# Kernel optimization log

Measured on AMD Instinct MI355X. Metric: run time of the kernel, lower is better.

Reference implementation:

```python
import jax, jax.numpy as jnp
import numpy as np
import math

B, S, IN_DIM, ORIG_DIM, EMBED, HEADS = 8, 1024, 512, 64, 512, 8
HEAD_DIM = EMBED // HEADS


def setup_inputs() -> dict:
    key = jax.random.key(0)
    ks = jax.random.split(key, 4)
    # xavier-uniform-ish init for weights, zero bias (matches _reset_parameters)
    def xavier(k, shape):
        fan_in, fan_out = shape[1], shape[0]
        lim = math.sqrt(6.0 / (fan_in + fan_out))
        return jax.random.uniform(k, shape, jnp.float32, -lim, lim)
    return {
        "x": jax.random.normal(ks[0], (B, S, IN_DIM), jnp.float32),
        "inp": jax.random.normal(ks[1], (B, S, ORIG_DIM), jnp.float32),
        "W_qkv": xavier(ks[2], (3 * EMBED, IN_DIM + ORIG_DIM)),
        "b_qkv": jnp.zeros((3 * EMBED,), jnp.float32),
        "W_o": xavier(ks[3], (EMBED, EMBED)),
        "b_o": jnp.zeros((EMBED,), jnp.float32),
    }


def reference(x, inp, W_qkv, b_qkv, W_o, b_o):
    b, s, _ = x.shape
    xc = jnp.concatenate([x, inp], axis=2)              # [B,S,IN+ORIG]
    qkv = xc @ W_qkv.T + b_qkv                          # [B,S,3E]
    qkv = qkv.reshape(b, s, HEADS, 3 * HEAD_DIM).transpose(0, 2, 1, 3)  # [B,H,S,3d]
    q, k, v = jnp.split(qkv, 3, axis=-1)                # each [B,H,S,d]
    logits = jnp.einsum("bhqd,bhkd->bhqk", q, k) / math.sqrt(HEAD_DIM)
    attention = jax.nn.softmax(logits, axis=-1)         # [B,H,S,S]
    values = jnp.einsum("bhqk,bhkd->bhqd", attention, v)
    values = values.transpose(0, 2, 1, 3).reshape(b, s, EMBED)
    o = values @ W_o.T + b_o                            # [B,S,E]
    return o, attention
```

## Files before the change

### kernel.cpp

```cpp
#include <hip/hip_runtime.h>

typedef __bf16 bf16x8 __attribute__((ext_vector_type(8)));
typedef __bf16 bf16x4 __attribute__((ext_vector_type(4)));
typedef float f32x4 __attribute__((ext_vector_type(4)));

#define MFMA16(a,b,c) __builtin_amdgcn_mfma_f32_16x16x32_bf16((a),(b),(c),0,0,0)

__device__ __forceinline__ float fexp2(float x) { return __builtin_amdgcn_exp2f(x); }

__device__ __forceinline__ void gload_lds16(const void* g, void* l) {
    __builtin_amdgcn_global_load_lds(
        (const __attribute__((address_space(1))) void*)g,
        (__attribute__((address_space(3))) void*)l, 16, 0, 0);
}


__global__ __launch_bounds__(256) void k_convert(
    const float* __restrict__ x, const float* __restrict__ inp,
    const float* __restrict__ Wqkv, const float* __restrict__ Wo,
    __bf16* __restrict__ xc, __bf16* __restrict__ wq, __bf16* __restrict__ wo)
{
    const unsigned C1 = 589824u;
    const unsigned C2 = 110592u;
    unsigned i = blockIdx.x * 256u + threadIdx.x;
    if (i < C1) {
        unsigned e = i * 8u;
        unsigned m = e / 576u, k = e - m * 576u;
        const float* p = (k < 512u) ? x + (size_t)m * 512u + k
                                    : inp + (size_t)m * 64u + (k - 512u);
        f32x4 a = *(const f32x4*)p, b = *(const f32x4*)(p + 4);
        bf16x8 o;
#pragma unroll
        for (int j = 0; j < 4; ++j) { o[j] = (__bf16)a[j]; o[j + 4] = (__bf16)b[j]; }
        *(bf16x8*)&xc[e] = o;
    } else if (i < C1 + C2) {
        unsigned e = (i - C1) * 8u;
        f32x4 a = *(const f32x4*)&Wqkv[e], b = *(const f32x4*)&Wqkv[e + 4];
        bf16x8 o;
#pragma unroll
        for (int j = 0; j < 4; ++j) { o[j] = (__bf16)a[j]; o[j + 4] = (__bf16)b[j]; }
        *(bf16x8*)&wq[e] = o;
    } else {
        unsigned e = (i - C1 - C2) * 8u;
        f32x4 a = *(const f32x4*)&Wo[e], b = *(const f32x4*)&Wo[e + 4];
        bf16x8 o;
#pragma unroll
        for (int j = 0; j < 4; ++j) { o[j] = (__bf16)a[j]; o[j + 4] = (__bf16)b[j]; }
        *(bf16x8*)&wo[e] = o;
    }
}

__global__ __launch_bounds__(256) void k_qkv_gemm(
    const __bf16* __restrict__ A, const __bf16* __restrict__ W,
    const float* __restrict__ bias,
    __bf16* __restrict__ q_ws, __bf16* __restrict__ k_ws, __bf16* __restrict__ vt_ws)
{
    const int K = 576;
    __shared__ __align__(16) char smem[17408];
    __bf16 (*As)[32] = (__bf16 (*)[32])smem;
    __bf16 (*Bs)[32] = (__bf16 (*)[32])(smem + 8192);
    int m0 = blockIdx.x * 128, n0 = blockIdx.y * 128;
    int t = threadIdx.x, w = t >> 6, l = t & 63;
    int lo = l & 15, hi = l >> 4;
    int wr = w >> 1, wc = w & 1;

    const __bf16* gA = A + (size_t)(m0 + w * 16 + (l >> 2)) * K + (l & 3) * 8;
    const __bf16* gB = W + (size_t)(n0 + w * 16 + (l >> 2)) * K + (l & 3) * 8;
    char* lA = smem + w * 1024;
    char* lB = smem + 8192 + w * 1024;

    float bias_reg[4];
#pragma unroll
    for (int ni = 0; ni < 4; ++ni) bias_reg[ni] = bias[n0 + wc * 64 + ni * 16 + lo];

    f32x4 acc[4][4] = {};
    for (int k0 = 0; k0 < K; k0 += 32) {
        gload_lds16(gA + k0, lA);
        gload_lds16(gA + 64 * K + k0, lA + 4096);
        gload_lds16(gB + k0, lB);
        gload_lds16(gB + 64 * K + k0, lB + 4096);
        __syncthreads();
        bf16x8 af[4], bq[4];
#pragma unroll
        for (int mi = 0; mi < 4; ++mi) af[mi] = *(const bf16x8*)&As[wr * 64 + mi * 16 + lo][hi * 8];
#pragma unroll
        for (int ni = 0; ni < 4; ++ni) bq[ni] = *(const bf16x8*)&Bs[wc * 64 + ni * 16 + lo][hi * 8];
#pragma unroll
        for (int mi = 0; mi < 4; ++mi)
#pragma unroll
            for (int ni = 0; ni < 4; ++ni)
                acc[mi][ni] = MFMA16(af[mi], bq[ni], acc[mi][ni]);
        __syncthreads();
    }

    int q64 = (n0 >> 6) + wc;
    int head = q64 / 3, part = q64 - head * 3;
    int mbase = m0 + wr * 64;
    size_t bh = (size_t)((mbase >> 10) * 8 + head);
    int sbase = mbase & 1023;

    if (part < 2) {
        float scale = (part == 0) ? 0.180336881f : 1.0f;
        __bf16* dst = (part == 0 ? q_ws : k_ws) + (bh * 1024 + sbase) * 64;
        __bf16 (*Ep)[68] = (__bf16 (*)[68])(smem + w * 4352);
#pragma unroll
        for (int hh = 0; hh < 2; ++hh) {
#pragma unroll
            for (int mi2 = 0; mi2 < 2; ++mi2) {
                int mi = hh * 2 + mi2;
#pragma unroll
                for (int ni = 0; ni < 4; ++ni)
#pragma unroll
                    for (int j = 0; j < 4; ++j)
                        Ep[mi2 * 16 + hi * 4 + j][ni * 16 + lo] =
                            (__bf16)((acc[mi][ni][j] + bias_reg[ni]) * scale);
            }
#pragma unroll
            for (int it = 0; it < 4; ++it) {
                int r = it * 8 + (l >> 3);
                bf16x8 v = *(const bf16x8*)&Ep[r][(l & 7) * 8];
                *(bf16x8*)&dst[(size_t)(hh * 32 + r) * 64 + (l & 7) * 8] = v;
            }
        }
    } else {
        __bf16* dst = vt_ws + bh * 65536 + sbase;
        __bf16 (*Ep)[34] = (__bf16 (*)[34])(smem + w * 4352);
#pragma unroll
        for (int hh = 0; hh < 2; ++hh) {
#pragma unroll
            for (int mi2 = 0; mi2 < 2; ++mi2) {
                int mi = hh * 2 + mi2;
#pragma unroll
                for (int ni = 0; ni < 4; ++ni)
#pragma unroll
                    for (int j = 0; j < 4; ++j)
                        Ep[ni * 16 + lo][mi2 * 16 + hi * 4 + j] =
                            (__bf16)(acc[mi][ni][j] + bias_reg[ni]);
            }
#pragma unroll
            for (int it = 0; it < 4; ++it) {
                int d = it * 16 + (l >> 2);
                bf16x8 v = *(const bf16x8*)&Ep[d][(l & 3) * 8];
                *(bf16x8*)&dst[(size_t)d * 1024 + hh * 32 + (l & 3) * 8] = v;
            }
        }
    }
}

__global__ __launch_bounds__(256, 4) void k_attn(
    const __bf16* __restrict__ q_ws, const __bf16* __restrict__ k_ws,
    const __bf16* __restrict__ vt_ws,
    float* __restrict__ att_out, __bf16* __restrict__ values)
{
    __shared__ __align__(16) __bf16 Klds[2][64][76];
    __shared__ __align__(16) __bf16 Pl[2][4][16][76];

    int bid = blockIdx.x;
    int nid = (bid & 7) * 128 + (bid >> 3);
    int bh = nid >> 4, qt = nid & 15;
    int t = threadIdx.x, w = t >> 6, l = t & 63;
    int lo = l & 15, hi = l >> 4;
    int q0 = qt * 64 + w * 16;

    const __bf16* Qg = q_ws + ((size_t)bh * 1024 + q0 + lo) * 64 + hi * 8;
    bf16x8 qa0 = *(const bf16x8*)Qg;
    bf16x8 qa1 = *(const bf16x8*)(Qg + 32);

    const __bf16* Kb = k_ws + (size_t)bh * 65536;
    int srow = t >> 2, scol = (t & 3) * 16;
    const __bf16* gK = Kb + (size_t)srow * 64 + scol;
    bf16x8 r0, r1;

#define STAGE_LOAD(c)  { const __bf16* p_ = gK + (size_t)(c) * 4096; \
                         r0 = *(const bf16x8*)p_; r1 = *(const bf16x8*)(p_ + 8); }
#define STAGE_WRITE(b) { *(bf16x8*)&Klds[b][srow][scol] = r0; \
                         *(bf16x8*)&Klds[b][srow][scol + 8] = r1; }
#define SCHUNK(b, s)   _Pragma("unroll") \
                       for (int kk = 0; kk < 4; ++kk) { \
                           bf16x8 kb0 = *(const bf16x8*)&Klds[b][kk * 16 + lo][hi * 8]; \
                           bf16x8 kb1 = *(const bf16x8*)&Klds[b][kk * 16 + lo][hi * 8 + 32]; \
                           f32x4 a_ = {}; \
                           a_ = MFMA16(qa0, kb0, a_); \
                           a_ = MFMA16(qa1, kb1, a_); \
                           s[kk] = a_; \
                       }

    f32x4 lmx = { -3.4e38f, -3.4e38f, -3.4e38f, -3.4e38f };
    f32x4 lsum = {};
    STAGE_LOAD(0); STAGE_WRITE(0);
    __syncthreads();
    for (int c = 0; c < 16; ++c) {
        if (c < 15) STAGE_LOAD(c + 1);
        f32x4 s[4];
        SCHUNK(c & 1, s);
#pragma unroll
        for (int j = 0; j < 4; ++j) {
            float cm = fmaxf(fmaxf(s[0][j], s[1][j]), fmaxf(s[2][j], s[3][j]));
            float nm = fmaxf(lmx[j], cm);
            float a = fexp2(s[0][j] - nm) + fexp2(s[1][j] - nm)
                    + fexp2(s[2][j] - nm) + fexp2(s[3][j] - nm);
            lsum[j] = lsum[j] * fexp2(lmx[j] - nm) + a;
            lmx[j] = nm;
        }
        if (c < 15) STAGE_WRITE((c + 1) & 1);
        __syncthreads();
    }
    f32x4 gmx = lmx;
#pragma unroll
    for (int off = 1; off < 16; off <<= 1)
#pragma unroll
        for (int j = 0; j < 4; ++j) gmx[j] = fmaxf(gmx[j], __shfl_xor(gmx[j], off));
    f32x4 part;
#pragma unroll
    for (int j = 0; j < 4; ++j) part[j] = lsum[j] * fexp2(lmx[j] - gmx[j]);
#pragma unroll
    for (int off = 1; off < 16; off <<= 1)
#pragma unroll
        for (int j = 0; j < 4; ++j) part[j] += __shfl_xor(part[j], off);
    f32x4 ginv;
#pragma unroll
    for (int j = 0; j < 4; ++j) ginv[j] = 1.f / part[j];

    float* gattW = att_out + ((size_t)bh * 1024 + q0) * 1024;
    const __bf16* Vb = vt_ws + (size_t)bh * 65536 + (size_t)(w * 16 + lo) * 1024 + hi * 8;
    f32x4 oacc[4] = {};

    STAGE_LOAD(0); STAGE_WRITE(0);
    __syncthreads();
    for (int c = 0; c < 16; ++c) {
        if (c < 15) STAGE_LOAD(c + 1);
        f32x4 s[4];
        SCHUNK(c & 1, s);
#pragma unroll
        for (int kk = 0; kk < 4; ++kk)
#pragma unroll
            for (int j = 0; j < 4; ++j) {
                float p = fexp2(s[kk][j] - gmx[j]) * ginv[j];
                gattW[(size_t)(hi * 4 + j) * 1024 + c * 64 + kk * 16 + lo] = p;
                Pl[c & 1][w][hi * 4 + j][kk * 16 + lo] = (__bf16)p;
            }
        if (c > 0) {
            int pb = (c - 1) & 1;
            const __bf16* vp = Vb + (size_t)(c - 1) * 64;
            bf16x8 vb0 = *(const bf16x8*)vp;
            bf16x8 vb1 = *(const bf16x8*)(vp + 32);
#pragma unroll
            for (int g = 0; g < 4; ++g) {
                bf16x8 pa0 = *(const bf16x8*)&Pl[pb][g][lo][hi * 8];
                bf16x8 pa1 = *(const bf16x8*)&Pl[pb][g][lo][hi * 8 + 32];
                oacc[g] = MFMA16(pa0, vb0, oacc[g]);
                oacc[g] = MFMA16(pa1, vb1, oacc[g]);
            }
        }
        if (c < 15) STAGE_WRITE((c + 1) & 1);
        __syncthreads();
    }
    {
        const __bf16* vp = Vb + (size_t)15 * 64;
        bf16x8 vb0 = *(const bf16x8*)vp;
        bf16x8 vb1 = *(const bf16x8*)(vp + 32);
#pragma unroll
        for (int g = 0; g < 4; ++g) {
            bf16x8 pa0 = *(const bf16x8*)&Pl[1][g][lo][hi * 8];
            bf16x8 pa1 = *(const bf16x8*)&Pl[1][g][lo][hi * 8 + 32];
            oacc[g] = MFMA16(pa0, vb0, oacc[g]);
            oacc[g] = MFMA16(pa1, vb1, oacc[g]);
        }
    }

    int b = bh >> 3, h = bh & 7;
#pragma unroll
    for (int g = 0; g < 4; ++g)
#pragma unroll
        for (int j = 0; j < 4; ++j)
            values[((size_t)b * 1024 + qt * 64 + g * 16 + hi * 4 + j) * 512
                   + h * 64 + w * 16 + lo] = (__bf16)oacc[g][j];
#undef STAGE_LOAD
#undef STAGE_WRITE
#undef SCHUNK
}

__global__ __launch_bounds__(256) void k_out_gemm(
    const __bf16* __restrict__ A, const __bf16* __restrict__ W,
    const float* __restrict__ bias, float* __restrict__ out)
{
    const int K = 512;
    __shared__ __align__(16) __bf16 As[128][32];
    __shared__ __align__(16) __bf16 Bs[128][32];
    int m0 = blockIdx.x * 128, n0 = blockIdx.y * 128;
    int t = threadIdx.x, w = t >> 6, l = t & 63;
    int lo = l & 15, hi = l >> 4;
    int wr = w >> 1, wc = w & 1;

    const __bf16* gA = A + (size_t)(m0 + w * 16 + (l >> 2)) * K + (l & 3) * 8;
    const __bf16* gB = W + (size_t)(n0 + w * 16 + (l >> 2)) * K + (l & 3) * 8;
    char* lA = (char*)&As[0][0] + w * 1024;
    char* lB = (char*)&Bs[0][0] + w * 1024;

    f32x4 acc[4][4] = {};
    for (int k0 = 0; k0 < K; k0 += 32) {
        gload_lds16(gA + k0, lA);
        gload_lds16(gA + 64 * K + k0, lA + 4096);
        gload_lds16(gB + k0, lB);
        gload_lds16(gB + 64 * K + k0, lB + 4096);
        __syncthreads();
        bf16x8 af[4], bq[4];
#pragma unroll
        for (int mi = 0; mi < 4; ++mi) af[mi] = *(const bf16x8*)&As[wr * 64 + mi * 16 + lo][hi * 8];
#pragma unroll
        for (int ni = 0; ni < 4; ++ni) bq[ni] = *(const bf16x8*)&Bs[wc * 64 + ni * 16 + lo][hi * 8];
#pragma unroll
        for (int mi = 0; mi < 4; ++mi)
#pragma unroll
            for (int ni = 0; ni < 4; ++ni)
                acc[mi][ni] = MFMA16(af[mi], bq[ni], acc[mi][ni]);
        __syncthreads();
    }

#pragma unroll
    for (int ni = 0; ni < 4; ++ni) {
        int n = n0 + wc * 64 + ni * 16 + lo;
        float bn = bias[n];
#pragma unroll
        for (int mi = 0; mi < 4; ++mi)
#pragma unroll
            for (int j = 0; j < 4; ++j) {
                int m = m0 + wr * 64 + mi * 16 + hi * 4 + j;
                out[(size_t)m * 512 + n] = acc[mi][ni][j] + bn;
            }
    }
}

extern "C" void kernel_launch(void* const* d_in, const int* in_sizes, int n_in,
                              void* d_out, int out_size, void* d_ws, size_t ws_size,
                              hipStream_t stream)
{
    const float* x    = (const float*)d_in[0];
    const float* inp  = (const float*)d_in[1];
    const float* Wqkv = (const float*)d_in[2];
    const float* bqkv = (const float*)d_in[3];
    const float* Wo   = (const float*)d_in[4];
    const float* bo   = (const float*)d_in[5];

    float* out_o   = (float*)d_out;
    float* out_att = out_o + (size_t)8 * 1024 * 512;

    char* ws = (char*)d_ws;
    __bf16* xc    = (__bf16*)(ws + 0);
    __bf16* wq    = (__bf16*)(ws + 9437184);
    __bf16* wo    = (__bf16*)(ws + 11206656);
    __bf16* q_ws  = (__bf16*)(ws + 11730944);
    __bf16* k_ws  = (__bf16*)(ws + 20119552);
    __bf16* vt_ws = (__bf16*)(ws + 28508160);
    __bf16* vals  = (__bf16*)(ws + 36896768);

    k_convert<<<2864, 256, 0, stream>>>(x, inp, Wqkv, Wo, xc, wq, wo);
    k_qkv_gemm<<<dim3(64, 12), 256, 0, stream>>>(xc, wq, bqkv, q_ws, k_ws, vt_ws);
    k_attn<<<1024, 256, 0, stream>>>(q_ws, k_ws, vt_ws, out_att, vals);
    k_out_gemm<<<dim3(64, 4), 256, 0, stream>>>(vals, wo, bo, out_o);
}
```

Baseline: 126.7 us.

## Double K-step per iteration and XOR-swizzle LDS tiles in QKV GEMM

The QKV projection GEMM now stages a 64-wide K slice per iteration instead of 32, which halves the number of barrier pairs, and grows LDS from about 17 KB to 32 KB. Tile rows are stored with an XOR swizzle on the 16-byte chunk index, applied on both the global-to-LDS load addresses and the fragment reads, to avoid LDS bank conflicts. The larger LDS footprint may lower occupancy, and K=576 must divide evenly by 64, which it does.

```diff
diff --git a/kernel.cpp b/kernel.cpp
--- a/kernel.cpp
+++ b/kernel.cpp
@@ -56,40 +56,51 @@
     __bf16* __restrict__ q_ws, __bf16* __restrict__ k_ws, __bf16* __restrict__ vt_ws)
 {
     const int K = 576;
-    __shared__ __align__(16) char smem[17408];
-    __bf16 (*As)[32] = (__bf16 (*)[32])smem;
-    __bf16 (*Bs)[32] = (__bf16 (*)[32])(smem + 8192);
+    __shared__ __align__(16) char smem[32768];
     int m0 = blockIdx.x * 128, n0 = blockIdx.y * 128;
     int t = threadIdx.x, w = t >> 6, l = t & 63;
     int lo = l & 15, hi = l >> 4;
     int wr = w >> 1, wc = w & 1;
 
-    const __bf16* gA = A + (size_t)(m0 + w * 16 + (l >> 2)) * K + (l & 3) * 8;
-    const __bf16* gB = W + (size_t)(n0 + w * 16 + (l >> 2)) * K + (l & 3) * 8;
-    char* lA = smem + w * 1024;
-    char* lB = smem + 8192 + w * 1024;
+    int srow = w * 8 + (l >> 3);
+    unsigned xswz = ((unsigned)((l & 7) * 16)) ^ (((unsigned)(l >> 3)) << 4);
+    const char* gA = (const char*)(A + (size_t)(m0 + srow) * K) + xswz;
+    const char* gB = (const char*)(W + (size_t)(n0 + srow) * K) + xswz;
 
     float bias_reg[4];
 #pragma unroll
     for (int ni = 0; ni < 4; ++ni) bias_reg[ni] = bias[n0 + wc * 64 + ni * 16 + lo];
 
+    unsigned xm = ((unsigned)(lo & 7)) << 4;
     f32x4 acc[4][4] = {};
-    for (int k0 = 0; k0 < K; k0 += 32) {
-        gload_lds16(gA + k0, lA);
-        gload_lds16(gA + 64 * K + k0, lA + 4096);
-        gload_lds16(gB + k0, lB);
-        gload_lds16(gB + 64 * K + k0, lB + 4096);
-        __syncthreads();
-        bf16x8 af[4], bq[4];
-#pragma unroll
-        for (int mi = 0; mi < 4; ++mi) af[mi] = *(const bf16x8*)&As[wr * 64 + mi * 16 + lo][hi * 8];
-#pragma unroll
-        for (int ni = 0; ni < 4; ++ni) bq[ni] = *(const bf16x8*)&Bs[wc * 64 + ni * 16 + lo][hi * 8];
-#pragma unroll
-        for (int mi = 0; mi < 4; ++mi)
-#pragma unroll
-            for (int ni = 0; ni < 4; ++ni)
-                acc[mi][ni] = MFMA16(af[mi], bq[ni], acc[mi][ni]);
+    for (int k0 = 0; k0 < K; k0 += 64) {
+#pragma unroll
+        for (int c = 0; c < 4; ++c) {
+            gload_lds16(gA + ((size_t)(32 * c) * K + k0) * 2, smem + c * 4096 + w * 1024);
+            gload_lds16(gB + ((size_t)(32 * c) * K + k0) * 2, smem + 16384 + c * 4096 + w * 1024);
+        }
+        __syncthreads();
+#pragma unroll
+        for (int ks = 0; ks < 2; ++ks) {
+            bf16x8 af[4], bq[4];
+#pragma unroll
+            for (int mi = 0; mi < 4; ++mi) {
+                int row = wr * 64 + mi * 16 + lo;
+                af[mi] = *(const bf16x8*)(smem + row * 128
+                          + (((unsigned)(ks * 64 + hi * 16)) ^ xm));
+            }
+#pragma unroll
+            for (int ni = 0; ni < 4; ++ni) {
+                int row = wc * 64 + ni * 16 + lo;
+                bq[ni] = *(const bf16x8*)(smem + 16384 + row * 128
+                          + (((unsigned)(ks * 64 + hi * 16)) ^ xm));
+            }
+#pragma unroll
+            for (int mi = 0; mi < 4; ++mi)
+#pragma unroll
+                for (int ni = 0; ni < 4; ++ni)
+                    acc[mi][ni] = MFMA16(af[mi], bq[ni], acc[mi][ni]);
+        }
         __syncthreads();
     }
 
```

Result: slower. 130.4 us (+2.9%).
